# Performance work log

Measured on AMD Instinct MI355X. Metric: run time of the kernel, lower is better.

Reference implementation:

```python
import jax, jax.numpy as jnp
import numpy as np


def log_g(x):
    # log of g(x) = where(x>=0, x+0.5, sigmoid(x))
    return jnp.where(x >= 0, jnp.log(jnp.maximum(x, 0) + 0.5), -jax.nn.softplus(-x))


def setup_inputs() -> dict:
    key = jax.random.key(0)
    ks = jax.random.split(key, 6)
    B, S, D, H = 4, 4096, 1024, 1024
    x = jax.random.normal(ks[0], (B, S, D), dtype=jnp.float32)
    h0 = jax.random.normal(ks[1], (B, 1, H), dtype=jnp.float32)
    # Linear params (scaled like trained weights to keep activations tame)
    Wz = jax.random.normal(ks[2], (H, D), dtype=jnp.float32) * 0.02
    bz = jax.random.normal(ks[3], (H,), dtype=jnp.float32) * 0.02
    Wh = jax.random.normal(ks[4], (H, D), dtype=jnp.float32) * 0.02
    bh = jax.random.normal(ks[5], (H,), dtype=jnp.float32) * 0.02
    return {"x": x, "h0": h0, "Wz": Wz, "bz": bz, "Wh": Wh, "bh": bh}


def reference(x, h0, Wz, bz, Wh, bh):
    # x: [B,S,D], h0: [B,1,H]
    k = jnp.einsum('bsd,hd->bsh', x, Wz) + bz            # linear_z(x)
    log_z = -jax.nn.softplus(-k)                          # log sigmoid(k)
    log_coeffs = -jax.nn.softplus(k)                      # log (1 - sigmoid(k))
    log_h0 = log_g(h0)                                    # [B,1,H]
    log_tilde_h = log_g(jnp.einsum('bsd,hd->bsh', x, Wh) + bh)
    log_coeffs = jnp.pad(log_coeffs, ((0, 0), (1, 0), (0, 0)))  # prepend zero coeff
    log_values = jnp.concatenate([log_h0, log_z + log_tilde_h], axis=1)  # [B,S+1,H]
    # parallel scan in log space
    a_star = jnp.cumsum(log_coeffs, axis=1)
    log_h = a_star + jax.lax.cumlogsumexp(log_values - a_star, axis=1)
    h = jnp.exp(log_h)
    out = h[:, 1:]                                        # last seq_len steps
    return (out, out[:, -1:])
```

## Files before the change

kernel.cpp:

```cpp
#include <hip/hip_runtime.h>
#include <hip/hip_bf16.h>
#include <stdint.h>

typedef __attribute__((ext_vector_type(4))) float f32x4;
typedef __attribute__((ext_vector_type(8))) short bf16x8;
typedef __attribute__((ext_vector_type(4))) unsigned short u16x4;
typedef __attribute__((ext_vector_type(4))) unsigned int u32x4;

constexpr int cB = 4, cS = 4096, cD = 1024, cH = 1024;
constexpr int cM = cB * cS;
constexpr int cK = cD;
constexpr int NCH = 64;
constexpr int CLEN = cS / NCH;

__device__ __forceinline__ unsigned short f2bf(float f) {
  union { float f; uint32_t u; } v; v.f = f;
  uint32_t r = v.u + 0x7FFFu + ((v.u >> 16) & 1u);
  return (unsigned short)(r >> 16);
}
__device__ __forceinline__ float bf2f(unsigned short h) {
  union { float f; uint32_t u; } v; v.u = ((uint32_t)h) << 16;
  return v.f;
}
__device__ __forceinline__ uint32_t pk2(float lo, float hi) {
  __hip_bfloat162 t = __float22bfloat162_rn(make_float2(lo, hi));
  union { __hip_bfloat162 b; uint32_t u; } v; v.b = t;
  return v.u;
}

__global__ void round_kernel(const float* __restrict__ src,
                             unsigned short* __restrict__ hi) {
  int i = (blockIdx.x * blockDim.x + threadIdx.x) * 4;
  f32x4 x = *(const f32x4*)(src + i);
  u16x4 h;
#pragma unroll
  for (int j = 0; j < 4; ++j) h[j] = f2bf(x[j]);
  *(u16x4*)(hi + i) = h;
}

constexpr int BM = 128, BN = 128, BK = 64;

__global__ __launch_bounds__(256, 2) void gemm_kernel(
    const float* __restrict__ xf,
    const unsigned short* __restrict__ wwh,
    const float* __restrict__ bz, const float* __restrict__ bhv,
    unsigned int* __restrict__ cgbuf,
    float* __restrict__ Pb, float* __restrict__ Qb)
{
  __shared__ unsigned short Ah[BM * BK], Bz[BN * BK], Bh[BN * BK];
  const int tid  = threadIdx.x;
  const int lane = tid & 63;
  const int wv   = tid >> 6;
  const int wr   = wv >> 1, wc = wv & 1;

  const int bid = blockIdx.x;
  const int xcd = bid & 7;
  const int idx = bid >> 3;
  const int mt  = xcd * 16 + (idx >> 3);
  const int nt  = idx & 7;
  const int m0 = mt * BM, n0 = nt * BN;
  const int fr = lane & 15, fq = lane >> 4;

  f32x4 accz[4][4] = {};
  f32x4 acch[4][4] = {};

  const int srow = tid >> 3;
  const int scol = (((tid & 7) ^ (srow & 7)) << 3);

  const float*          gX = xf  + (size_t)m0 * cK;
  const unsigned short* gZ = wwh + (size_t)n0 * cK;
  const unsigned short* gH = wwh + (size_t)(cH + n0) * cK;

  for (int kt = 0; kt < cK / BK; ++kt) {
    const int k0 = kt * BK;
    __syncthreads();
#pragma unroll
    for (int r = 0; r < 4; ++r) {
      const int row = r * 32 + srow;
      const int ldsoff = r * 4096 + tid * 16;
      const size_t goff = (size_t)row * cK + k0 + scol;
      __builtin_amdgcn_global_load_lds((const __attribute__((address_space(1))) void*)(gZ + goff),
        (__attribute__((address_space(3))) void*)((char*)Bz + ldsoff), 16, 0, 0);
      __builtin_amdgcn_global_load_lds((const __attribute__((address_space(1))) void*)(gH + goff),
        (__attribute__((address_space(3))) void*)((char*)Bh + ldsoff), 16, 0, 0);
    }
#pragma unroll
    for (int r = 0; r < 4; ++r) {
      const int row = r * 32 + srow;
      const int ldsoff = r * 4096 + tid * 16;
      const size_t goff = (size_t)row * cK + k0 + scol;
      const f32x4 alo = *(const f32x4*)(gX + goff);
      const f32x4 ahi = *(const f32x4*)(gX + goff + 4);
      u32x4 apk;
      apk[0] = pk2(alo[0], alo[1]);
      apk[1] = pk2(alo[2], alo[3]);
      apk[2] = pk2(ahi[0], ahi[1]);
      apk[3] = pk2(ahi[2], ahi[3]);
      *(u32x4*)((char*)Ah + ldsoff) = apk;
    }
    __syncthreads();
#pragma unroll
    for (int kk = 0; kk < BK / 32; ++kk) {
      bf16x8 fa[4], fz[4], fh[4];
#pragma unroll
      for (int i = 0; i < 4; ++i) {
        const int ar = wr * 64 + i * 16 + fr;
        const int ca = (kk * 64 + fq * 16) ^ ((ar & 7) << 4);
        fa[i] = *(const bf16x8*)((const char*)Ah + ar * 128 + ca);
        const int br = wc * 64 + i * 16 + fr;
        const int cb = (kk * 64 + fq * 16) ^ ((br & 7) << 4);
        fz[i] = *(const bf16x8*)((const char*)Bz + br * 128 + cb);
        fh[i] = *(const bf16x8*)((const char*)Bh + br * 128 + cb);
      }
#pragma unroll
      for (int i = 0; i < 4; ++i)
#pragma unroll
        for (int j = 0; j < 4; ++j) {
          accz[i][j] = __builtin_amdgcn_mfma_f32_16x16x32_bf16(fa[i], fz[j], accz[i][j], 0, 0, 0);
          acch[i][j] = __builtin_amdgcn_mfma_f32_16x16x32_bf16(fa[i], fh[j], acch[i][j], 0, 0, 0);
        }
    }
  }

  const int b  = mt >> 5;
  const int ch = (mt & 31) * 2 + wr;
#pragma unroll
  for (int j = 0; j < 4; ++j) {
    const int n = n0 + wc * 64 + j * 16 + fr;
    const float bz_n = bz[n];
    const float bh_n = bhv[n];
    float psg[4], qsg[4];
#pragma unroll
    for (int i = 0; i < 4; ++i) {
      float p = 1.0f, q = 0.0f;
#pragma unroll
      for (int rg = 0; rg < 4; ++rg) {
        const int m = m0 + wr * 64 + i * 16 + fq * 4 + rg;
        const float kv = accz[i][j][rg] + bz_n;
        const float av = acch[i][j][rg] + bh_n;
        const float c = 1.0f / (1.0f + __expf(kv));
        const float g = (av >= 0.0f) ? (av + 0.5f) : (1.0f / (1.0f + __expf(-av)));
        cgbuf[(size_t)m * cH + n] = pk2(c, g);
        q = c * q + (1.0f - c) * g;
        p = c * p;
      }
      float pp = __shfl_xor(p, 16), qq = __shfl_xor(q, 16);
      if (fq & 1) { q = q + p * qq; } else { q = qq + pp * q; }
      p = p * pp;
      pp = __shfl_xor(p, 32); qq = __shfl_xor(q, 32);
      if (fq & 2) { q = q + p * qq; } else { q = qq + pp * q; }
      p = p * pp;
      psg[i] = p; qsg[i] = q;
    }
    float P = psg[0], Q = qsg[0];
#pragma unroll
    for (int i = 1; i < 4; ++i) { Q = qsg[i] + psg[i] * Q; P = psg[i] * P; }
    if (fq == 0) {
      const size_t o = ((size_t)b * NCH + ch) * cH + n;
      Pb[o] = P; Qb[o] = Q;
    }
  }
}

__global__ void scan_prefix_kernel(const float* __restrict__ h0,
                                   const float* __restrict__ Pb, const float* __restrict__ Qb,
                                   float* __restrict__ hin) {
  const int wid  = (blockIdx.x * blockDim.x + threadIdx.x) >> 6;
  const int lane = threadIdx.x & 63;
  const int b = wid >> 10, h = wid & 1023;
  const size_t o = ((size_t)b * NCH + lane) * cH + h;
  float P = Pb[o], Q = Qb[o];
#pragma unroll
  for (int off = 1; off < 64; off <<= 1) {
    float Po = __shfl_up(P, off), Qo = __shfl_up(Q, off);
    if (lane >= off) { Q = P * Qo + Q; P = P * Po; }
  }
  float Pe = __shfl_up(P, 1), Qe = __shfl_up(Q, 1);
  if (lane == 0) { Pe = 1.0f; Qe = 0.0f; }
  const float x = h0[b * cH + h];
  const float h0g = (x >= 0.0f) ? (x + 0.5f) : (1.0f / (1.0f + expf(-x)));
  hin[o] = Pe * h0g + Qe;
}

__global__ void scan_write_kernel(const unsigned int* __restrict__ cg,
                                  const float* __restrict__ hin, float* __restrict__ out) {
  const int bc = blockIdx.x;
  const int b = bc / NCH, ch = bc % NCH;
  const int h4 = threadIdx.x * 4;
  f32x4 hc = *(const f32x4*)(hin + ((size_t)b * NCH + ch) * cH + h4);
  size_t base = ((size_t)b * cS + (size_t)ch * CLEN) * cH + h4;
#pragma unroll 4
  for (int i = 0; i < CLEN; ++i) {
    u32x4 v = *(const u32x4*)(cg + base + (size_t)i * cH);
#pragma unroll
    for (int j = 0; j < 4; ++j) {
      const float c = bf2f((unsigned short)(v[j] & 0xFFFFu));
      const float g = bf2f((unsigned short)(v[j] >> 16));
      hc[j] = c * hc[j] + (1.0f - c) * g;
    }
    *(f32x4*)(out + base + (size_t)i * cH) = hc;
  }
  if (ch == NCH - 1) {
    *(f32x4*)(out + (size_t)cM * cH + (size_t)b * cH + h4) = hc;
  }
}

extern "C" void kernel_launch(void* const* d_in, const int* in_sizes, int n_in,
                              void* d_out, int out_size, void* d_ws, size_t ws_size,
                              hipStream_t stream) {
  const float* x   = (const float*)d_in[0];
  const float* h0  = (const float*)d_in[1];
  const float* Wz  = (const float*)d_in[2];
  const float* bz  = (const float*)d_in[3];
  const float* Wh  = (const float*)d_in[4];
  const float* bh  = (const float*)d_in[5];

  char* ws = (char*)d_ws;
  unsigned short* wwh  = (unsigned short*)(ws + (((size_t)32) << 20));
  unsigned int*   cgbuf= (unsigned int*)(ws + (((size_t)40) << 20));
  float* Pb   = (float*)(ws + (((size_t)104) << 20));
  float* Qb   = (float*)(ws + (((size_t)105) << 20));
  float* hin  = (float*)(ws + (((size_t)106) << 20));
  float* out  = (float*)d_out;

  round_kernel<<<cH * cK / 1024, 256, 0, stream>>>(Wz, wwh);
  round_kernel<<<cH * cK / 1024, 256, 0, stream>>>(Wh, wwh + (size_t)cH * cK);
  gemm_kernel<<<(cM / BM) * (cH / BN), 256, 0, stream>>>(x, wwh, bz, bh, cgbuf, Pb, Qb);
  scan_prefix_kernel<<<cB * cH * 64 / 256, 256, 0, stream>>>(h0, Pb, Qb, hin);
  scan_write_kernel<<<cB * NCH, 256, 0, stream>>>(cgbuf, hin, out);
}
```

Before: 126.3 us.

## Double-buffer weight tiles in LDS and prefetch next k-tile during MFMA

Measured after the change: 117.7 us (median of 2 runs). 1.07x faster.

```diff
diff --git a/kernel.cpp b/kernel.cpp
--- a/kernel.cpp
+++ b/kernel.cpp
@@ -28,17 +28,22 @@
   return v.u;
 }
 
-__global__ void round_kernel(const float* __restrict__ src,
-                             unsigned short* __restrict__ hi) {
-  int i = (blockIdx.x * blockDim.x + threadIdx.x) * 4;
-  f32x4 x = *(const f32x4*)(src + i);
+__global__ void roundW_kernel(const float* __restrict__ wz, const float* __restrict__ wh,
+                              unsigned short* __restrict__ dst) {
+  const int nb = (cH * cK) / 1024;
+  const int bidx = blockIdx.x;
+  const bool second = (bidx >= nb);
+  const float* src = second ? wh : wz;
+  const int base = ((second ? bidx - nb : bidx) * 256 + threadIdx.x) * 4;
+  f32x4 x = *(const f32x4*)(src + base);
   u16x4 h;
 #pragma unroll
   for (int j = 0; j < 4; ++j) h[j] = f2bf(x[j]);
-  *(u16x4*)(hi + i) = h;
+  *(u16x4*)(dst + (second ? cH * cK : 0) + base) = h;
 }
 
 constexpr int BM = 128, BN = 128, BK = 64;
+constexpr int NT = cK / BK;
 
 __global__ __launch_bounds__(256, 2) void gemm_kernel(
     const float* __restrict__ xf,
@@ -47,7 +52,9 @@
     unsigned int* __restrict__ cgbuf,
     float* __restrict__ Pb, float* __restrict__ Qb)
 {
-  __shared__ unsigned short Ah[BM * BK], Bz[BN * BK], Bh[BN * BK];
+  __shared__ unsigned short Ah[BM * BK];
+  __shared__ unsigned short Bzb[2][BN * BK];
+  __shared__ unsigned short Bhb[2][BN * BK];
   const int tid  = threadIdx.x;
   const int lane = tid & 63;
   const int wv   = tid >> 6;
@@ -71,34 +78,49 @@
   const unsigned short* gZ = wwh + (size_t)n0 * cK;
   const unsigned short* gH = wwh + (size_t)(cH + n0) * cK;
 
-  for (int kt = 0; kt < cK / BK; ++kt) {
+#pragma unroll
+  for (int r = 0; r < 4; ++r) {
+    const int ldsoff = r * 4096 + tid * 16;
+    const size_t goff = (size_t)(r * 32 + srow) * cK + scol;
+    __builtin_amdgcn_global_load_lds((const __attribute__((address_space(1))) void*)(gZ + goff),
+      (__attribute__((address_space(3))) void*)((char*)Bzb[0] + ldsoff), 16, 0, 0);
+    __builtin_amdgcn_global_load_lds((const __attribute__((address_space(1))) void*)(gH + goff),
+      (__attribute__((address_space(3))) void*)((char*)Bhb[0] + ldsoff), 16, 0, 0);
+  }
+
+  for (int kt = 0; kt < NT; ++kt) {
+    const int cur = kt & 1, nxt = cur ^ 1;
     const int k0 = kt * BK;
-    __syncthreads();
+    f32x4 av[8];
 #pragma unroll
     for (int r = 0; r < 4; ++r) {
-      const int row = r * 32 + srow;
-      const int ldsoff = r * 4096 + tid * 16;
-      const size_t goff = (size_t)row * cK + k0 + scol;
-      __builtin_amdgcn_global_load_lds((const __attribute__((address_space(1))) void*)(gZ + goff),
-        (__attribute__((address_space(3))) void*)((char*)Bz + ldsoff), 16, 0, 0);
-      __builtin_amdgcn_global_load_lds((const __attribute__((address_space(1))) void*)(gH + goff),
-        (__attribute__((address_space(3))) void*)((char*)Bh + ldsoff), 16, 0, 0);
-    }
+      const size_t goff = (size_t)(r * 32 + srow) * cK + k0 + scol;
+      av[2 * r]     = *(const f32x4*)(gX + goff);
+      av[2 * r + 1] = *(const f32x4*)(gX + goff + 4);
+    }
+    if (kt + 1 < NT) {
+      const int kn = k0 + BK;
+#pragma unroll
+      for (int r = 0; r < 4; ++r) {
+        const int ldsoff = r * 4096 + tid * 16;
+        const size_t goff = (size_t)(r * 32 + srow) * cK + kn + scol;
+        __builtin_amdgcn_global_load_lds((const __attribute__((address_space(1))) void*)(gZ + goff),
+          (__attribute__((address_space(3))) void*)((char*)Bzb[nxt] + ldsoff), 16, 0, 0);
+        __builtin_amdgcn_global_load_lds((const __attribute__((address_space(1))) void*)(gH + goff),
+          (__attribute__((address_space(3))) void*)((char*)Bhb[nxt] + ldsoff), 16, 0, 0);
+      }
+    }
+    asm volatile("s_waitcnt vmcnt(8)" ::: "memory");
 #pragma unroll
     for (int r = 0; r < 4; ++r) {
-      const int row = r * 32 + srow;
-      const int ldsoff = r * 4096 + tid * 16;
-      const size_t goff = (size_t)row * cK + k0 + scol;
-      const f32x4 alo = *(const f32x4*)(gX + goff);
-      const f32x4 ahi = *(const f32x4*)(gX + goff + 4);
       u32x4 apk;
-      apk[0] = pk2(alo[0], alo[1]);
-      apk[1] = pk2(alo[2], alo[3]);
-      apk[2] = pk2(ahi[0], ahi[1]);
-      apk[3] = pk2(ahi[2], ahi[3]);
-      *(u32x4*)((char*)Ah + ldsoff) = apk;
-    }
-    __syncthreads();
+      apk[0] = pk2(av[2 * r][0], av[2 * r][1]);
+      apk[1] = pk2(av[2 * r][2], av[2 * r][3]);
+      apk[2] = pk2(av[2 * r + 1][0], av[2 * r + 1][1]);
+      apk[3] = pk2(av[2 * r + 1][2], av[2 * r + 1][3]);
+      *(u32x4*)((char*)Ah + r * 4096 + tid * 16) = apk;
+    }
+    asm volatile("s_waitcnt lgkmcnt(0)\n\ts_barrier" ::: "memory");
 #pragma unroll
     for (int kk = 0; kk < BK / 32; ++kk) {
       bf16x8 fa[4], fz[4], fh[4];
@@ -109,8 +131,8 @@
         fa[i] = *(const bf16x8*)((const char*)Ah + ar * 128 + ca);
         const int br = wc * 64 + i * 16 + fr;
         const int cb = (kk * 64 + fq * 16) ^ ((br & 7) << 4);
-        fz[i] = *(const bf16x8*)((const char*)Bz + br * 128 + cb);
-        fh[i] = *(const bf16x8*)((const char*)Bh + br * 128 + cb);
+        fz[i] = *(const bf16x8*)((const char*)Bzb[cur] + br * 128 + cb);
+        fh[i] = *(const bf16x8*)((const char*)Bhb[cur] + br * 128 + cb);
       }
 #pragma unroll
       for (int i = 0; i < 4; ++i)
@@ -120,6 +142,7 @@
           acch[i][j] = __builtin_amdgcn_mfma_f32_16x16x32_bf16(fa[i], fh[j], acch[i][j], 0, 0, 0);
         }
     }
+    asm volatile("s_barrier" ::: "memory");
   }
 
   const int b  = mt >> 5;
@@ -137,9 +160,10 @@
       for (int rg = 0; rg < 4; ++rg) {
         const int m = m0 + wr * 64 + i * 16 + fq * 4 + rg;
         const float kv = accz[i][j][rg] + bz_n;
-        const float av = acch[i][j][rg] + bh_n;
-        const float c = 1.0f / (1.0f + __expf(kv));
-        const float g = (av >= 0.0f) ? (av + 0.5f) : (1.0f / (1.0f + __expf(-av)));
+        const float av2 = acch[i][j][rg] + bh_n;
+        const float c = __builtin_amdgcn_rcpf(1.0f + __expf(kv));
+        const float g = (av2 >= 0.0f) ? (av2 + 0.5f)
+                                      : __builtin_amdgcn_rcpf(1.0f + __expf(-av2));
         cgbuf[(size_t)m * cH + n] = pk2(c, g);
         q = c * q + (1.0f - c) * g;
         p = c * p;
@@ -223,8 +247,7 @@
   float* hin  = (float*)(ws + (((size_t)106) << 20));
   float* out  = (float*)d_out;
 
-  round_kernel<<<cH * cK / 1024, 256, 0, stream>>>(Wz, wwh);
-  round_kernel<<<cH * cK / 1024, 256, 0, stream>>>(Wh, wwh + (size_t)cH * cK);
+  roundW_kernel<<<2 * cH * cK / 1024, 256, 0, stream>>>(Wz, Wh, wwh);
   gemm_kernel<<<(cM / BM) * (cH / BN), 256, 0, stream>>>(x, wwh, bz, bh, cgbuf, Pb, Qb);
   scan_prefix_kernel<<<cB * cH * 64 / 256, 256, 0, stream>>>(h0, Pb, Qb, hin);
   scan_write_kernel<<<cB * NCH, 256, 0, stream>>>(cgbuf, hin, out);
```
